# Kernel tuning notes

Measured on AMD Instinct MI355X. Metric: run time of the kernel, lower is better.

Reference implementation:

```python
import jax, jax.numpy as jnp
import numpy as np

IN_N, IN_D, OUT_N, OUT_D = 2048, 16, 64, 16
LN_EPS = 1e-5

def setup_inputs() -> dict:
    key = jax.random.key(0)
    k1, k2 = jax.random.split(key)
    w_const = np.sqrt(OUT_N / (IN_D * IN_N)).astype(np.float32)
    return {
        "input": jax.random.normal(k1, (128, IN_N, IN_D), dtype=jnp.float32),
        "w": w_const * jax.random.normal(k2, (IN_N, IN_D, OUT_N, OUT_D), dtype=jnp.float32),
        "ln_gamma": jnp.ones((OUT_D,), dtype=jnp.float32),
        "ln_beta": jnp.zeros((OUT_D,), dtype=jnp.float32),
    }

def _squash(x):
    # squash along last dim: (|x|^2/(1+|x|^2)) * x/|x|
    sq = jnp.sum(x * x, axis=-1, keepdims=True)
    return (sq / (1.0 + sq)) * x / jnp.sqrt(sq)

def reference(input, w, ln_gamma, ln_beta):
    b, n, a = input.shape
    m = w.shape[2]
    # query_key=None path: softmax over zeros -> uniform 1/m routing coeffs
    qk = jnp.full((n, m), 1.0 / m, dtype=input.dtype)
    # bmd = sum_{n,a} qk[n,m] * input[b,n,a] * w[n,a,m,d]
    v = jnp.einsum('nm,bna,namd->bmd', qk, input, w)
    v = _squash(v)
    new_qk = jnp.einsum('bna,namd,bmd->bnm', input, w, v)
    # dropout with p=0 (eval) is identity; LayerNorm over out_d_capsules
    mu = jnp.mean(v, axis=-1, keepdims=True)
    var = jnp.mean((v - mu) ** 2, axis=-1, keepdims=True)
    v = (v - mu) / jnp.sqrt(var + LN_EPS) * ln_gamma + ln_beta
    return (new_qk, v)
```

## Files before the change

kernel.cpp:

```cpp
#include <hip/hip_runtime.h>
#include <cstdint>
#include <cstddef>

typedef short bfrag  __attribute__((ext_vector_type(8)));
typedef float facc   __attribute__((ext_vector_type(4)));
typedef float f32x16 __attribute__((ext_vector_type(16)));
typedef float f32x4v __attribute__((ext_vector_type(4)));

namespace {
constexpr int B = 128, N = 2048, A = 16, M = 64, D = 16;
constexpr int NA = N * A;
constexpr int MD = M * D;
constexpr size_t C_ELEMS = (size_t)B * MD;
constexpr int WP = 24;
}

static __device__ __forceinline__ ushort f2bf(float x) {
    uint u = __float_as_uint(x);
    u += 0x7fffu + ((u >> 16) & 1u);
    return (ushort)(u >> 16);
}
static __device__ __forceinline__ bfrag ld_frag16(const ushort* p) {
    union { uint4 q; bfrag v; } u;
    u.q = *(const uint4*)p;
    return u.v;
}
static __device__ __forceinline__ bfrag ld_frag4(const ushort* p) {
    const uint* q = (const uint*)p;
    union { uint a[4]; bfrag v; } u;
    u.a[0] = q[0]; u.a[1] = q[1]; u.a[2] = q[2]; u.a[3] = q[3];
    return u.v;
}

__global__ __launch_bounds__(512, 2) void k1_mfma(const float* __restrict__ in,
                                                  const float* __restrict__ w,
                                                  float* __restrict__ part,
                                                  int nch) {
    const int mdg   = blockIdx.x;
    const int chunk = blockIdx.y;
    const int t     = threadIdx.x;
    const int nap   = NA / nch;
    const int nkt   = nap / 64;
    __shared__ __align__(16) ushort in_t[128 * 72];
    __shared__ __align__(16) ushort w_t[256 * 66];
    const int wv = t >> 6, tl = t & 63;
    const int wb = wv >> 2, wm = wv & 3;
    const int lr = tl & 15, hi = tl >> 4;

    facc acc[4][4];
    #pragma unroll
    for (int i = 0; i < 4; ++i)
        #pragma unroll
        for (int j = 0; j < 4; ++j) acc[i][j] = facc{0.f, 0.f, 0.f, 0.f};

    float4 pin[4], pw[8];
    const int ib  = t >> 4, ik = t & 15;
    const int wk  = t >> 6, wmd = t & 63;

    int na0 = (size_t)chunk * nap;
    #pragma unroll
    for (int q = 0; q < 4; ++q)
        pin[q] = *(const float4*)(in + (size_t)(q * 32 + ib) * NA + na0 + ik * 4);
    #pragma unroll
    for (int q = 0; q < 8; ++q)
        pw[q] = *(const float4*)(w + (size_t)(na0 + q * 8 + wk) * MD + mdg * 256 + wmd * 4);

    for (int kt = 0; kt < nkt; ++kt) {
        __syncthreads();
        #pragma unroll
        for (int q = 0; q < 4; ++q) {
            union { ushort s[4]; uint2 u; } pk;
            pk.s[0] = f2bf(pin[q].x); pk.s[1] = f2bf(pin[q].y);
            pk.s[2] = f2bf(pin[q].z); pk.s[3] = f2bf(pin[q].w);
            *(uint2*)(&in_t[(q * 32 + ib) * 72 + ik * 4]) = pk.u;
        }
        #pragma unroll
        for (int q = 0; q < 8; ++q) {
            const int krow = q * 8 + wk;
            w_t[(wmd * 4 + 0) * 66 + krow] = f2bf(pw[q].x);
            w_t[(wmd * 4 + 1) * 66 + krow] = f2bf(pw[q].y);
            w_t[(wmd * 4 + 2) * 66 + krow] = f2bf(pw[q].z);
            w_t[(wmd * 4 + 3) * 66 + krow] = f2bf(pw[q].w);
        }
        __syncthreads();
        if (kt + 1 < nkt) {
            const int nan = na0 + 64;
            #pragma unroll
            for (int q = 0; q < 4; ++q)
                pin[q] = *(const float4*)(in + (size_t)(q * 32 + ib) * NA + nan + ik * 4);
            #pragma unroll
            for (int q = 0; q < 8; ++q)
                pw[q] = *(const float4*)(w + (size_t)(nan + q * 8 + wk) * MD + mdg * 256 + wmd * 4);
        }
        #pragma unroll
        for (int ks = 0; ks < 2; ++ks) {
            bfrag af[4], bf[4];
            #pragma unroll
            for (int bt = 0; bt < 4; ++bt)
                af[bt] = ld_frag16(&in_t[(wb * 64 + bt * 16 + lr) * 72 + ks * 32 + hi * 8]);
            #pragma unroll
            for (int mt = 0; mt < 4; ++mt)
                bf[mt] = ld_frag4(&w_t[(wm * 64 + mt * 16 + lr) * 66 + ks * 32 + hi * 8]);
            #pragma unroll
            for (int bt = 0; bt < 4; ++bt)
                #pragma unroll
                for (int mt = 0; mt < 4; ++mt)
                    acc[bt][mt] = __builtin_amdgcn_mfma_f32_16x16x32_bf16(
                        af[bt], bf[mt], acc[bt][mt], 0, 0, 0);
        }
        na0 += 64;
    }
    #pragma unroll
    for (int bt = 0; bt < 4; ++bt)
        #pragma unroll
        for (int mt = 0; mt < 4; ++mt) {
            const int b  = wb * 64 + bt * 16 + hi * 4;
            const int md = mdg * 256 + wm * 64 + mt * 16 + lr;
            #pragma unroll
            for (int r = 0; r < 4; ++r)
                part[((size_t)chunk * B + b + r) * MD + md] = acc[bt][mt][r];
        }
}

__global__ __launch_bounds__(256) void k2_squash_ln(const float* __restrict__ part,
                                                    const float* __restrict__ gamma,
                                                    const float* __restrict__ beta,
                                                    float* __restrict__ v_sq,
                                                    float* __restrict__ out_v,
                                                    int nch) {
    const int idx = blockIdx.x * 256 + threadIdx.x;
    const int d   = idx & 15;
    float s = 0.f;
    for (int c = 0; c < nch; ++c) s += part[(size_t)c * C_ELEMS + idx];
    const float v = s * (1.0f / 64.0f);
    float sq = v * v;
    #pragma unroll
    for (int off = 1; off < 16; off <<= 1) sq += __shfl_xor(sq, off, 16);
    const float f  = sqrtf(sq) / (1.0f + sq);
    const float vs = v * f;
    v_sq[idx] = vs;
    float mu = vs;
    #pragma unroll
    for (int off = 1; off < 16; off <<= 1) mu += __shfl_xor(mu, off, 16);
    mu *= (1.0f / 16.0f);
    const float dd = vs - mu;
    float var = dd * dd;
    #pragma unroll
    for (int off = 1; off < 16; off <<= 1) var += __shfl_xor(var, off, 16);
    var *= (1.0f / 16.0f);
    out_v[idx] = dd / sqrtf(var + 1e-5f) * gamma[d] + beta[d];
}

__global__ __launch_bounds__(512, 4) void k3_mfma3(const float* __restrict__ in,
                                                   const float* __restrict__ w,
                                                   const float* __restrict__ vsq,
                                                   float* __restrict__ qk) {
    const int m0 = blockIdx.x * 8;
    const int n0 = blockIdx.y * 16;
    const int t  = threadIdx.x;
    const int wv = t >> 6;
    const int nh = wv >> 2, bg = wv & 3;
    const int lane = t & 63;
    const int lc = lane & 31, l5 = lane >> 5;
    const int b  = bg * 32 + lc;

    __shared__ __align__(16) ushort wt[2][2][4 * 32 * WP];
    __shared__ __align__(16) ushort it[2][2][128 * WP];

    f32x4v vr[8][2];
    #pragma unroll
    for (int mm = 0; mm < 8; ++mm) {
        vr[mm][0] = *(const f32x4v*)(vsq + ((size_t)b * M + m0 + mm) * D + 4 * l5);
        vr[mm][1] = *(const f32x4v*)(vsq + ((size_t)b * M + m0 + mm) * D + 8 + 4 * l5);
    }

    const int s_nn = t >> 8, r = t & 255;
    const int wa1 = r & 7, wd4 = (r >> 3) & 3, wm_ = r >> 5;
    const int ib_ = r >> 1, iq = r & 1;

    float4 pw[2], pi[2];
    auto ldg = [&](int ph) {
        const int n = n0 + ph * 2 + s_nn;
        #pragma unroll
        for (int j = 0; j < 2; ++j)
            pw[j] = *(const float4*)(
                w + ((size_t)(n * A + wa1 * 2 + j) * M + m0 + wm_) * D + wd4 * 4);
        #pragma unroll
        for (int j = 0; j < 2; ++j)
            pi[j] = *(const float4*)(in + (size_t)ib_ * NA + n * A + iq * 8 + j * 4);
    };
    auto stg = [&](int p) {
        ushort* wb_ = &wt[p][s_nn][((wm_ >> 1) * 32 + (wm_ & 1) * 16) * WP];
        #pragma unroll
        for (int k = 0; k < 4; ++k) {
            union { ushort s[2]; uint u; } v;
            v.s[0] = f2bf(pw[0][k]);
            v.s[1] = f2bf(pw[1][k]);
            *(uint*)(&wb_[(wd4 * 4 + k) * WP + wa1 * 2]) = v.u;
        }
        union { ushort s[8]; uint4 q; } pk;
        #pragma unroll
        for (int j = 0; j < 2; ++j) {
            pk.s[j * 4 + 0] = f2bf(pi[j].x); pk.s[j * 4 + 1] = f2bf(pi[j].y);
            pk.s[j * 4 + 2] = f2bf(pi[j].z); pk.s[j * 4 + 3] = f2bf(pi[j].w);
        }
        *(uint4*)(&it[p][s_nn][ib_ * WP + iq * 8]) = pk.q;
    };

    ldg(0);
    stg(0);
    ldg(1);
    __syncthreads();

    for (int ph = 0; ph < 8; ++ph) {
        const int p = ph & 1;
        if (ph < 7) stg(p ^ 1);
        if (ph < 6) ldg(ph + 2);

        const int n = n0 + ph * 2 + nh;
        const bfrag bf = ld_frag16(&it[p][nh][b * WP + l5 * 8]);
        float out4[4];
        #pragma unroll
        for (int mp = 0; mp < 4; ++mp) {
            const bfrag af = ld_frag16(&wt[p][nh][(mp * 32 + lc) * WP + l5 * 8]);
            f32x16 c = {};
            c = __builtin_amdgcn_mfma_f32_32x32x16_bf16(af, bf, c, 0, 0, 0);
            #pragma unroll
            for (int mj = 0; mj < 2; ++mj) {
                float s = 0.f;
                #pragma unroll
                for (int rr = 0; rr < 8; ++rr)
                    s += c[mj * 8 + rr] * vr[mp * 2 + mj][rr >> 2][rr & 3];
                s += __shfl_xor(s, 32);
                if ((mp >> 1) == l5) out4[(mp & 1) * 2 + mj] = s;
            }
        }
        const float4 o = {out4[0], out4[1], out4[2], out4[3]};
        *(float4*)(qk + ((size_t)b * N + n) * M + m0 + l5 * 4) = o;
        __syncthreads();
    }
}

extern "C" void kernel_launch(void* const* d_in, const int* in_sizes, int n_in,
                              void* d_out, int out_size, void* d_ws, size_t ws_size,
                              hipStream_t stream) {
    const float* in    = (const float*)d_in[0];
    const float* w     = (const float*)d_in[1];
    const float* gamma = (const float*)d_in[2];
    const float* beta  = (const float*)d_in[3];
    float* out_qk = (float*)d_out;
    float* out_v  = out_qk + (size_t)B * N * M;

    int nch = 64;
    if (ws_size < (64 + 1) * C_ELEMS * sizeof(float)) nch = 16;
    if (ws_size < (16 + 1) * C_ELEMS * sizeof(float)) nch = 8;
    float* part = (float*)d_ws;
    float* vsq  = part + (size_t)nch * C_ELEMS;

    k1_mfma<<<dim3(4, nch), 512, 0, stream>>>(in, w, part, nch);
    k2_squash_ln<<<(int)(C_ELEMS / 256), 256, 0, stream>>>(part, gamma, beta, vsq, out_v, nch);
    k3_mfma3<<<dim3(8, 128), 512, 0, stream>>>(in, w, vsq, out_qk);
}
```

Baseline: 135.8 us.

## Reuse bf16-converted weights and inputs from first pass in direct third kernel

The first GEMM kernel now writes its LDS-staged bf16 transposed weight tile to a workspace buffer, and a new pre-kernel converts the input to bf16. A new third kernel reads these bf16 buffers straight from global memory in MFMA fragment order with register double-buffering, so it skips the fp32 reload, the conversion and the LDS staging and barriers of the old k3. The cost is extra global writes (a 64 MB bf16 weight copy plus the input copy), a fourth launch, and more workspace, with a fallback to the old path when workspace is too small.

```diff
diff --git a/kernel.cpp b/kernel.cpp
--- a/kernel.cpp
+++ b/kernel.cpp
@@ -12,7 +12,6 @@
 constexpr int NA = N * A;
 constexpr int MD = M * D;
 constexpr size_t C_ELEMS = (size_t)B * MD;
-constexpr int WP = 24;
 }
 
 static __device__ __forceinline__ ushort f2bf(float x) {
@@ -32,10 +31,22 @@
     return u.v;
 }
 
+__global__ __launch_bounds__(256) void k0_cvt(const float* __restrict__ in,
+                                              ushort* __restrict__ inb) {
+    const size_t i = (size_t)blockIdx.x * 256 + threadIdx.x;
+    const float4 a = *(const float4*)(in + i * 8);
+    const float4 c = *(const float4*)(in + i * 8 + 4);
+    union { ushort s[8]; uint4 q; } p;
+    p.s[0] = f2bf(a.x); p.s[1] = f2bf(a.y); p.s[2] = f2bf(a.z); p.s[3] = f2bf(a.w);
+    p.s[4] = f2bf(c.x); p.s[5] = f2bf(c.y); p.s[6] = f2bf(c.z); p.s[7] = f2bf(c.w);
+    *(uint4*)(inb + i * 8) = p.q;
+}
+
 __global__ __launch_bounds__(512, 2) void k1_mfma(const float* __restrict__ in,
                                                   const float* __restrict__ w,
                                                   float* __restrict__ part,
-                                                  int nch) {
+                                                  ushort* __restrict__ wT,
+                                                  int nch, int dump) {
     const int mdg   = blockIdx.x;
     const int chunk = blockIdx.y;
     const int t     = threadIdx.x;
@@ -57,7 +68,7 @@
     const int ib  = t >> 4, ik = t & 15;
     const int wk  = t >> 6, wmd = t & 63;
 
-    int na0 = (size_t)chunk * nap;
+    int na0 = chunk * nap;
     #pragma unroll
     for (int q = 0; q < 4; ++q)
         pin[q] = *(const float4*)(in + (size_t)(q * 32 + ib) * NA + na0 + ik * 4);
@@ -91,6 +102,18 @@
             #pragma unroll
             for (int q = 0; q < 8; ++q)
                 pw[q] = *(const float4*)(w + (size_t)(nan + q * 8 + wk) * MD + mdg * 256 + wmd * 4);
+        }
+        if (dump) {
+            const int mdl = t >> 1, kh = t & 1;
+            const uint* s32 = (const uint*)&w_t[mdl * 66 + kh * 32];
+            ushort* dst = wT + (size_t)(mdg * 256 + mdl) * NA + na0 + kh * 32;
+            #pragma unroll
+            for (int j = 0; j < 4; ++j) {
+                uint4 o;
+                o.x = s32[j * 4]; o.y = s32[j * 4 + 1];
+                o.z = s32[j * 4 + 2]; o.w = s32[j * 4 + 3];
+                *(uint4*)(dst + j * 8) = o;
+            }
         }
         #pragma unroll
         for (int ks = 0; ks < 2; ++ks) {
@@ -151,10 +174,71 @@
     out_v[idx] = dd / sqrtf(var + 1e-5f) * gamma[d] + beta[d];
 }
 
+__global__ __launch_bounds__(256) void k3_direct(const ushort* __restrict__ wT,
+                                                 const ushort* __restrict__ inb,
+                                                 const float* __restrict__ vsq,
+                                                 float* __restrict__ qk) {
+    const int m0 = blockIdx.x * 8;
+    const int n0 = blockIdx.y * 32;
+    const int t  = threadIdx.x;
+    const int wv = t >> 6, lane = t & 63;
+    const int lc = lane & 31, l5 = lane >> 5;
+    const int b  = wv * 32 + lc;
+
+    f32x4v vr[8][2];
+    #pragma unroll
+    for (int mm = 0; mm < 8; ++mm) {
+        vr[mm][0] = *(const f32x4v*)(vsq + ((size_t)b * M + m0 + mm) * D + 4 * l5);
+        vr[mm][1] = *(const f32x4v*)(vsq + ((size_t)b * M + m0 + mm) * D + 8 + 4 * l5);
+    }
+    const ushort* arow = wT + ((size_t)(m0 + (lc >> 4)) * 16 + (lc & 15)) * NA + l5 * 8;
+    const ushort* brow = inb + (size_t)b * NA + l5 * 8;
+
+    bfrag ac0, ac1, ac2, ac3, bc;
+    ac0 = ld_frag16(arow + (size_t)0 * 32 * NA + n0 * 16);
+    ac1 = ld_frag16(arow + (size_t)1 * 32 * NA + n0 * 16);
+    ac2 = ld_frag16(arow + (size_t)2 * 32 * NA + n0 * 16);
+    ac3 = ld_frag16(arow + (size_t)3 * 32 * NA + n0 * 16);
+    bc  = ld_frag16(brow + n0 * 16);
+
+    for (int i = 0; i < 32; ++i) {
+        bfrag an0, an1, an2, an3, bn;
+        if (i + 1 < 32) {
+            const int nx = (n0 + i + 1) * 16;
+            an0 = ld_frag16(arow + (size_t)0 * 32 * NA + nx);
+            an1 = ld_frag16(arow + (size_t)1 * 32 * NA + nx);
+            an2 = ld_frag16(arow + (size_t)2 * 32 * NA + nx);
+            an3 = ld_frag16(arow + (size_t)3 * 32 * NA + nx);
+            bn  = ld_frag16(brow + nx);
+        }
+        const int n = n0 + i;
+        float out4[4];
+        bfrag aa[4] = {ac0, ac1, ac2, ac3};
+        #pragma unroll
+        for (int mp = 0; mp < 4; ++mp) {
+            f32x16 c = {};
+            c = __builtin_amdgcn_mfma_f32_32x32x16_bf16(aa[mp], bc, c, 0, 0, 0);
+            #pragma unroll
+            for (int mj = 0; mj < 2; ++mj) {
+                float s = 0.f;
+                #pragma unroll
+                for (int rr = 0; rr < 8; ++rr)
+                    s += c[mj * 8 + rr] * vr[mp * 2 + mj][rr >> 2][rr & 3];
+                s += __shfl_xor(s, 32);
+                if ((mp >> 1) == l5) out4[(mp & 1) * 2 + mj] = s;
+            }
+        }
+        *(float4*)(qk + ((size_t)b * N + n) * M + m0 + l5 * 4) =
+            float4{out4[0], out4[1], out4[2], out4[3]};
+        if (i + 1 < 32) { ac0 = an0; ac1 = an1; ac2 = an2; ac3 = an3; bc = bn; }
+    }
+}
+
 __global__ __launch_bounds__(512, 4) void k3_mfma3(const float* __restrict__ in,
                                                    const float* __restrict__ w,
                                                    const float* __restrict__ vsq,
                                                    float* __restrict__ qk) {
+    constexpr int WP = 24;
     const int m0 = blockIdx.x * 8;
     const int n0 = blockIdx.y * 16;
     const int t  = threadIdx.x;
@@ -163,21 +247,17 @@
     const int lane = t & 63;
     const int lc = lane & 31, l5 = lane >> 5;
     const int b  = bg * 32 + lc;
-
     __shared__ __align__(16) ushort wt[2][2][4 * 32 * WP];
     __shared__ __align__(16) ushort it[2][2][128 * WP];
-
     f32x4v vr[8][2];
     #pragma unroll
     for (int mm = 0; mm < 8; ++mm) {
         vr[mm][0] = *(const f32x4v*)(vsq + ((size_t)b * M + m0 + mm) * D + 4 * l5);
         vr[mm][1] = *(const f32x4v*)(vsq + ((size_t)b * M + m0 + mm) * D + 8 + 4 * l5);
     }
-
     const int s_nn = t >> 8, r = t & 255;
     const int wa1 = r & 7, wd4 = (r >> 3) & 3, wm_ = r >> 5;
     const int ib_ = r >> 1, iq = r & 1;
-
     float4 pw[2], pi[2];
     auto ldg = [&](int ph) {
         const int n = n0 + ph * 2 + s_nn;
@@ -206,17 +286,12 @@
         }
         *(uint4*)(&it[p][s_nn][ib_ * WP + iq * 8]) = pk.q;
     };
-
-    ldg(0);
-    stg(0);
-    ldg(1);
+    ldg(0); stg(0); ldg(1);
     __syncthreads();
-
     for (int ph = 0; ph < 8; ++ph) {
         const int p = ph & 1;
         if (ph < 7) stg(p ^ 1);
         if (ph < 6) ldg(ph + 2);
-
         const int n = n0 + ph * 2 + nh;
         const bfrag bf = ld_frag16(&it[p][nh][b * WP + l5 * 8]);
         float out4[4];
@@ -235,8 +310,8 @@
                 if ((mp >> 1) == l5) out4[(mp & 1) * 2 + mj] = s;
             }
         }
-        const float4 o = {out4[0], out4[1], out4[2], out4[3]};
-        *(float4*)(qk + ((size_t)b * N + n) * M + m0 + l5 * 4) = o;
+        *(float4*)(qk + ((size_t)b * N + n) * M + m0 + l5 * 4) =
+            float4{out4[0], out4[1], out4[2], out4[3]};
         __syncthreads();
     }
 }
@@ -251,13 +326,36 @@
     float* out_qk = (float*)d_out;
     float* out_v  = out_qk + (size_t)B * N * M;
 
+    const size_t WT_BYTES = (size_t)MD * NA * 2;
+    const size_t IN_BYTES = (size_t)B * NA * 2;
+    auto need = [&](int nc) {
+        return (size_t)(nc + 1) * C_ELEMS * 4 + WT_BYTES + IN_BYTES;
+    };
     int nch = 64;
-    if (ws_size < (64 + 1) * C_ELEMS * sizeof(float)) nch = 16;
-    if (ws_size < (16 + 1) * C_ELEMS * sizeof(float)) nch = 8;
-    float* part = (float*)d_ws;
-    float* vsq  = part + (size_t)nch * C_ELEMS;
-
-    k1_mfma<<<dim3(4, nch), 512, 0, stream>>>(in, w, part, nch);
-    k2_squash_ln<<<(int)(C_ELEMS / 256), 256, 0, stream>>>(part, gamma, beta, vsq, out_v, nch);
-    k3_mfma3<<<dim3(8, 128), 512, 0, stream>>>(in, w, vsq, out_qk);
-}
+    bool direct = true;
+    if (ws_size < need(64)) nch = 16;
+    if (ws_size < need(16)) nch = 8;
+    if (ws_size < need(8)) {
+        direct = false;
+        nch = 64;
+        if (ws_size < (64 + 1) * C_ELEMS * sizeof(float)) nch = 16;
+        if (ws_size < (16 + 1) * C_ELEMS * sizeof(float)) nch = 8;
+    }
+    float*  part = (float*)d_ws;
+    float*  vsq  = part + (size_t)nch * C_ELEMS;
+    ushort* wT   = (ushort*)(vsq + C_ELEMS);
+    ushort* inb  = wT + (size_t)MD * NA;
+
+    if (direct) {
+        k0_cvt<<<2048, 256, 0, stream>>>(in, inb);
+        k1_mfma<<<dim3(4, nch), 512, 0, stream>>>(in, w, part, wT, nch, 1);
+        k2_squash_ln<<<(int)(C_ELEMS / 256), 256, 0, stream>>>(part, gamma, beta,
+                                                               vsq, out_v, nch);
+        k3_direct<<<dim3(8, 64), 256, 0, stream>>>(wT, inb, vsq, out_qk);
+    } else {
+        k1_mfma<<<dim3(4, nch), 512, 0, stream>>>(in, w, part, wT, nch, 0);
+        k2_squash_ln<<<(int)(C_ELEMS / 256), 256, 0, stream>>>(part, gamma, beta,
+                                                               vsq, out_v, nch);
+        k3_mfma3<<<dim3(8, 128), 512, 0, stream>>>(in, w, vsq, out_qk);
+    }
+}
```

Result: slower. 157.9 us (+16.3%).
